# Kernel tuning notes

Hardware: AMD Instinct MI355X
Metric: run time of the kernel (lower is better)

## Reference

```python
import jax, jax.numpy as jnp
import numpy as np

B, SQ, SKV, D = 16, 2048, 2048, 128


def setup_inputs() -> dict:
    key = jax.random.key(0)
    kq, kk, kv = jax.random.split(key, 3)
    q = jax.random.normal(kq, (B, SQ, D), dtype=jnp.float32)
    k = jax.random.normal(kk, (B, SKV, D), dtype=jnp.float32)
    v = jax.random.normal(kv, (B, SKV, D), dtype=jnp.float32)
    return {"q": q, "k": k, "v": v, "dropout_p": 0}


def reference(q, k, v, dropout_p):
    # scores = q @ k^T, scaled by 1/sqrt(d)
    scale = 1.0 / np.sqrt(q.shape[-1]).astype(np.float32)
    scores = jnp.einsum('bqd,bkd->bqk', q, k) * scale  # [B, SQ, SKV]
    attn = jax.nn.softmax(scores, axis=-1)
    # dropout with p=dropout_p (0 here -> identity; deterministic baseline)
    if dropout_p > 0:
        keep = 1.0 - dropout_p
        mask = jax.random.bernoulli(jax.random.key(42), keep, attn.shape)
        attn = jnp.where(mask, attn / keep, 0.0)
    return jnp.einsum('bqk,bkd->bqd', attn, v)
```

## Files before the change

### kernel.cpp

```cpp
#include <hip/hip_runtime.h>
#include <hip/hip_bf16.h>
#include <cstdint>
#include <cmath>

#define SQL 2048
#define SKVL 2048
#define DD 128
#define NB 16
#define QBLK 64
#define KVB 32
#define NT 32

typedef __attribute__((ext_vector_type(8))) short short8;
typedef __attribute__((ext_vector_type(4))) float f32x4;

__device__ __forceinline__ ushort f2bf(float x) {
    union { float f; uint32_t u; } v; v.f = x;
    uint32_t r = v.u + 0x7FFFu + ((v.u >> 16) & 1u);
    return (ushort)(r >> 16);
}

__global__ void convert_scale_k(const float* __restrict__ in, ushort* __restrict__ out, float scale) {
    size_t i = (size_t)blockIdx.x * blockDim.x + threadIdx.x;
    const f32x4* p = (const f32x4*)in + i * 2;
    f32x4 a = p[0], b = p[1];
    short8 o;
    o[0] = (short)f2bf(a[0] * scale);
    o[1] = (short)f2bf(a[1] * scale);
    o[2] = (short)f2bf(a[2] * scale);
    o[3] = (short)f2bf(a[3] * scale);
    o[4] = (short)f2bf(b[0] * scale);
    o[5] = (short)f2bf(b[1] * scale);
    o[6] = (short)f2bf(b[2] * scale);
    o[7] = (short)f2bf(b[3] * scale);
    *((short8*)out + i) = o;
}

__global__ void convert_k_tiled(const float* __restrict__ in, ushort* __restrict__ out) {
    int gid = blockIdx.x * blockDim.x + threadIdx.x;
    int c16 = gid & 15;
    int rg  = gid >> 4;
    int r   = rg & 31;
    int tile = rg >> 5;
    const f32x4* p = (const f32x4*)(in + (size_t)rg * DD + c16 * 8);
    f32x4 a = p[0], b = p[1];
    short8 o;
    o[0] = (short)f2bf(a[0]); o[1] = (short)f2bf(a[1]);
    o[2] = (short)f2bf(a[2]); o[3] = (short)f2bf(a[3]);
    o[4] = (short)f2bf(b[0]); o[5] = (short)f2bf(b[1]);
    o[6] = (short)f2bf(b[2]); o[7] = (short)f2bf(b[3]);
    int cs = c16 ^ (r & 7);
    *(short8*)(out + ((size_t)tile << 12) + r * 128 + cs * 8) = o;
}

__global__ void convert_vt_tiled(const float* __restrict__ v, ushort* __restrict__ vt) {
    __shared__ float tile[32][129];
    int bid = blockIdx.x;
    int kt = bid & 63;
    int b  = bid >> 6;
    int tx = threadIdx.x;
    const float* src = v + ((size_t)b * SKVL + (size_t)kt * 32) * DD;
#pragma unroll
    for (int i = 0; i < 16; ++i) {
        int e = i * 256 + tx;
        tile[e >> 7][e & 127] = src[e];
    }
    __syncthreads();
    ushort* dst = vt + ((size_t)bid << 12);
#pragma unroll
    for (int i = 0; i < 2; ++i) {
        int q = i * 256 + tx;
        int d = q >> 2;
        int csp = q & 3;
        int cs = csp ^ ((d >> 1) & 3);
        short8 o;
#pragma unroll
        for (int j = 0; j < 8; ++j) {
            int kv = (j >> 2) * 16 + cs * 4 + (j & 3);
            o[j] = (short)f2bf(tile[kv][d]);
        }
        *(short8*)(dst + d * 32 + csp * 8) = o;
    }
}

#define GLD_LDS16(gsrc, ldst) \
    __builtin_amdgcn_global_load_lds((const __attribute__((address_space(1))) uint32_t*)(gsrc), \
                                     (__attribute__((address_space(3))) uint32_t*)(ldst), 16, 0, 0)

__global__ __launch_bounds__(256, 2) void fattn(
    const ushort* __restrict__ qb, const ushort* __restrict__ kbt,
    const ushort* __restrict__ vbt, float* __restrict__ out)
{
    __shared__ short8 kls[2][2][512];
    __shared__ short8 vls[2][2][512];

    int bid = blockIdx.x;
    int swz = (bid & 7) * 64 + (bid >> 3);
    int b  = swz >> 5;
    int qt = swz & 31;
    int lane = threadIdx.x & 63;
    int w = threadIdx.x >> 6;
    int g = lane >> 4;
    int qi = lane & 15;
    int rx = qi & 7;
    int vx = g ^ ((qi >> 1) & 3);
    int qrow = qt * QBLK + w * 16 + qi;

    const char* kA = (const char*)(kbt + ((size_t)(b * 64) << 12));
    const char* vA = (const char*)(vbt + ((size_t)(b * 64) << 12));
    const char* kB = kA + ((size_t)NT << 13);
    const char* vB = vA + ((size_t)NT << 13);

    const ushort* qptr = qb + ((size_t)b * SQL + qrow) * DD;
    short8 qf[4];
#pragma unroll
    for (int ks = 0; ks < 4; ++ks)
        qf[ks] = *(const short8*)(qptr + ks * 32 + g * 8);

    f32x4 accA[8], accB[8];
#pragma unroll
    for (int i = 0; i < 8; ++i) { accA[i] = (f32x4)0.f; accB[i] = (f32x4)0.f; }
    float mA = -1e30f, lA = 0.f, mB = -1e30f, lB = 0.f;

#pragma unroll
    for (int i = 0; i < 2; ++i) {
        int off = w * 2048 + i * 1024;
        GLD_LDS16(kA + off + lane * 16, (char*)&kls[0][0][0] + off);
        GLD_LDS16(vA + off + lane * 16, (char*)&vls[0][0][0] + off);
        GLD_LDS16(kB + off + lane * 16, (char*)&kls[1][0][0] + off);
        GLD_LDS16(vB + off + lane * 16, (char*)&vls[1][0][0] + off);
    }
    __syncthreads();

    for (int t = 0; t < NT; ++t) {
        int cur = t & 1, nxt = cur ^ 1;
        if (t + 1 < NT) {
            size_t toff = (size_t)(t + 1) << 13;
#pragma unroll
            for (int i = 0; i < 2; ++i) {
                int off = w * 2048 + i * 1024;
                GLD_LDS16(kA + toff + off + lane * 16, (char*)&kls[0][nxt][0] + off);
                GLD_LDS16(vA + toff + off + lane * 16, (char*)&vls[0][nxt][0] + off);
                GLD_LDS16(kB + toff + off + lane * 16, (char*)&kls[1][nxt][0] + off);
                GLD_LDS16(vB + toff + off + lane * 16, (char*)&vls[1][nxt][0] + off);
            }
        }
#pragma unroll
        for (int s2 = 0; s2 < 2; ++s2) {
            f32x4* acc = s2 ? accB : accA;
            float& m = s2 ? mB : mA;
            float& lsum = s2 ? lB : lA;
            f32x4 st[2];
            __builtin_amdgcn_s_setprio(1);
#pragma unroll
            for (int sub = 0; sub < 2; ++sub) {
                f32x4 s = (f32x4)0.f;
                int r = sub * 16 + qi;
#pragma unroll
                for (int ks = 0; ks < 4; ++ks) {
                    short8 kf = kls[s2][cur][r * 16 + ((ks * 4 + g) ^ rx)];
                    s = __builtin_amdgcn_mfma_f32_16x16x32_bf16(kf, qf[ks], s, 0, 0, 0);
                }
                st[sub] = s;
            }
            __builtin_amdgcn_s_setprio(0);
            float m0 = fmaxf(fmaxf(st[0][0], st[0][1]), fmaxf(st[0][2], st[0][3]));
            float m1 = fmaxf(fmaxf(st[1][0], st[1][1]), fmaxf(st[1][2], st[1][3]));
            float vmax = fmaxf(m0, m1);
            if (__any(vmax > m + 11.5f)) {
                float tmax = fmaxf(vmax, __shfl_xor(vmax, 16));
                tmax = fmaxf(tmax, __shfl_xor(tmax, 32));
                float mnew = fmaxf(m, tmax);
                float alpha = exp2f(m - mnew);
                m = mnew;
                lsum *= alpha;
#pragma unroll
                for (int i = 0; i < 8; ++i) {
                    acc[i][0] *= alpha; acc[i][1] *= alpha;
                    acc[i][2] *= alpha; acc[i][3] *= alpha;
                }
            }
            float pvv[8];
#pragma unroll
            for (int s = 0; s < 2; ++s) {
                pvv[s * 4 + 0] = exp2f(st[s][0] - m);
                pvv[s * 4 + 1] = exp2f(st[s][1] - m);
                pvv[s * 4 + 2] = exp2f(st[s][2] - m);
                pvv[s * 4 + 3] = exp2f(st[s][3] - m);
            }
            lsum += ((pvv[0] + pvv[1]) + (pvv[2] + pvv[3])) + ((pvv[4] + pvv[5]) + (pvv[6] + pvv[7]));
            union { short8 v; uint32_t u[4]; } P;
#pragma unroll
            for (int i = 0; i < 4; ++i)
                asm("v_cvt_pk_bf16_f32 %0, %1, %2" : "=v"(P.u[i]) : "v"(pvv[2 * i]), "v"(pvv[2 * i + 1]));
            __builtin_amdgcn_s_setprio(1);
#pragma unroll
            for (int dt = 0; dt < 8; ++dt) {
                int d = dt * 16 + qi;
                acc[dt] = __builtin_amdgcn_mfma_f32_16x16x32_bf16(
                    vls[s2][cur][d * 4 + vx], P.v, acc[dt], 0, 0, 0);
            }
            __builtin_amdgcn_s_setprio(0);
        }
        __syncthreads();
    }

    float mf = fmaxf(mA, mB);
    float fa = exp2f(mA - mf), fb = exp2f(mB - mf);
    float l = lA * fa + lB * fb;
    l += __shfl_xor(l, 16);
    l += __shfl_xor(l, 32);
    float inv = 1.f / l;
    float fia = fa * inv, fib = fb * inv;
    float* optr = out + ((size_t)b * SQL + qrow) * DD + g * 4;
#pragma unroll
    for (int dt = 0; dt < 8; ++dt) {
        f32x4 o;
        o[0] = accA[dt][0] * fia + accB[dt][0] * fib;
        o[1] = accA[dt][1] * fia + accB[dt][1] * fib;
        o[2] = accA[dt][2] * fia + accB[dt][2] * fib;
        o[3] = accA[dt][3] * fia + accB[dt][3] * fib;
        *(f32x4*)(optr + dt * 16) = o;
    }
}

extern "C" void kernel_launch(void* const* d_in, const int* in_sizes, int n_in,
                              void* d_out, int out_size, void* d_ws, size_t ws_size,
                              hipStream_t stream) {
    const float* q = (const float*)d_in[0];
    const float* k = (const float*)d_in[1];
    const float* v = (const float*)d_in[2];
    float* out = (float*)d_out;

    uint8_t* w = (uint8_t*)d_ws;
    size_t tsz = (size_t)NB * SQL * DD * sizeof(ushort);
    ushort* qb  = (ushort*)w;
    ushort* kbt = (ushort*)(w + tsz);
    ushort* vbt = (ushort*)(w + 2 * tsz);

    float qscale = 1.4426950408889634f / sqrtf((float)DD);
    int n8 = NB * SQL * DD / 8;
    convert_scale_k<<<n8 / 256, 256, 0, stream>>>(q, qb, qscale);
    convert_k_tiled<<<NB * SKVL * 16 / 256, 256, 0, stream>>>(k, kbt);
    convert_vt_tiled<<<NB * (SKVL / 32), 256, 0, stream>>>(v, vbt);
    fattn<<<NB * (SQL / QBLK), 256, 0, stream>>>(qb, kbt, vbt, out);
}
```

Baseline: 155.8 us.

## Split KV halves across separate warp groups with 512-thread blocks and LDS merge

```diff
diff --git a/kernel.cpp b/kernel.cpp
--- a/kernel.cpp
+++ b/kernel.cpp
@@ -87,7 +87,7 @@
     __builtin_amdgcn_global_load_lds((const __attribute__((address_space(1))) uint32_t*)(gsrc), \
                                      (__attribute__((address_space(3))) uint32_t*)(ldst), 16, 0, 0)
 
-__global__ __launch_bounds__(256, 2) void fattn(
+__global__ __launch_bounds__(512, 4) void fattn(
     const ushort* __restrict__ qb, const ushort* __restrict__ kbt,
     const ushort* __restrict__ vbt, float* __restrict__ out)
 {
@@ -100,16 +100,26 @@
     int qt = swz & 31;
     int lane = threadIdx.x & 63;
     int w = threadIdx.x >> 6;
+    int s2 = w >> 2;
+    int qg = w & 3;
     int g = lane >> 4;
     int qi = lane & 15;
     int rx = qi & 7;
     int vx = g ^ ((qi >> 1) & 3);
-    int qrow = qt * QBLK + w * 16 + qi;
-
-    const char* kA = (const char*)(kbt + ((size_t)(b * 64) << 12));
-    const char* vA = (const char*)(vbt + ((size_t)(b * 64) << 12));
-    const char* kB = kA + ((size_t)NT << 13);
-    const char* vB = vA + ((size_t)NT << 13);
+    int qrow = qt * QBLK + qg * 16 + qi;
+
+    const char* kS0 = (const char*)(kbt + ((size_t)(b * 64) << 12));
+    const char* vS0 = (const char*)(vbt + ((size_t)(b * 64) << 12));
+    const char* kS1 = kS0 + ((size_t)NT << 13);
+    const char* vS1 = vS0 + ((size_t)NT << 13);
+
+    int rreg = w >> 1;
+    const char* gbase = (rreg == 0) ? kS0 : (rreg == 1) ? vS0 : (rreg == 2) ? kS1 : vS1;
+    char* l0 = (rreg == 0) ? (char*)kls[0][0] : (rreg == 1) ? (char*)vls[0][0]
+             : (rreg == 2) ? (char*)kls[1][0] : (char*)vls[1][0];
+    char* l1 = (rreg == 0) ? (char*)kls[0][1] : (rreg == 1) ? (char*)vls[0][1]
+             : (rreg == 2) ? (char*)kls[1][1] : (char*)vls[1][1];
+    int soff = (w & 1) * 4096;
 
     const ushort* qptr = qb + ((size_t)b * SQL + qrow) * DD;
     short8 qf[4];
@@ -117,110 +127,115 @@
     for (int ks = 0; ks < 4; ++ks)
         qf[ks] = *(const short8*)(qptr + ks * 32 + g * 8);
 
-    f32x4 accA[8], accB[8];
-#pragma unroll
-    for (int i = 0; i < 8; ++i) { accA[i] = (f32x4)0.f; accB[i] = (f32x4)0.f; }
-    float mA = -1e30f, lA = 0.f, mB = -1e30f, lB = 0.f;
-
-#pragma unroll
-    for (int i = 0; i < 2; ++i) {
-        int off = w * 2048 + i * 1024;
-        GLD_LDS16(kA + off + lane * 16, (char*)&kls[0][0][0] + off);
-        GLD_LDS16(vA + off + lane * 16, (char*)&vls[0][0][0] + off);
-        GLD_LDS16(kB + off + lane * 16, (char*)&kls[1][0][0] + off);
-        GLD_LDS16(vB + off + lane * 16, (char*)&vls[1][0][0] + off);
-    }
+    f32x4 acc[8];
+#pragma unroll
+    for (int i = 0; i < 8; ++i) acc[i] = (f32x4)0.f;
+    float m = -1e30f, lsum = 0.f;
+
+#pragma unroll
+    for (int i = 0; i < 4; ++i)
+        GLD_LDS16(gbase + soff + i * 1024 + lane * 16, l0 + soff + i * 1024);
     __syncthreads();
+
+    const short8* kst = kls[s2][0];
+    const short8* vst = vls[s2][0];
 
     for (int t = 0; t < NT; ++t) {
         int cur = t & 1, nxt = cur ^ 1;
         if (t + 1 < NT) {
             size_t toff = (size_t)(t + 1) << 13;
-#pragma unroll
-            for (int i = 0; i < 2; ++i) {
-                int off = w * 2048 + i * 1024;
-                GLD_LDS16(kA + toff + off + lane * 16, (char*)&kls[0][nxt][0] + off);
-                GLD_LDS16(vA + toff + off + lane * 16, (char*)&vls[0][nxt][0] + off);
-                GLD_LDS16(kB + toff + off + lane * 16, (char*)&kls[1][nxt][0] + off);
-                GLD_LDS16(vB + toff + off + lane * 16, (char*)&vls[1][nxt][0] + off);
+            char* ld = nxt ? l1 : l0;
+#pragma unroll
+            for (int i = 0; i < 4; ++i)
+                GLD_LDS16(gbase + toff + soff + i * 1024 + lane * 16, ld + soff + i * 1024);
+        }
+        const short8* kcur = kst + cur * 512;
+        const short8* vcur = vst + cur * 512;
+        f32x4 st[2];
+        __builtin_amdgcn_s_setprio(1);
+#pragma unroll
+        for (int sub = 0; sub < 2; ++sub) {
+            f32x4 s = (f32x4)0.f;
+            int r = sub * 16 + qi;
+#pragma unroll
+            for (int ks = 0; ks < 4; ++ks) {
+                short8 kf = kcur[r * 16 + ((ks * 4 + g) ^ rx)];
+                s = __builtin_amdgcn_mfma_f32_16x16x32_bf16(kf, qf[ks], s, 0, 0, 0);
             }
-        }
-#pragma unroll
-        for (int s2 = 0; s2 < 2; ++s2) {
-            f32x4* acc = s2 ? accB : accA;
-            float& m = s2 ? mB : mA;
-            float& lsum = s2 ? lB : lA;
-            f32x4 st[2];
-            __builtin_amdgcn_s_setprio(1);
-#pragma unroll
-            for (int sub = 0; sub < 2; ++sub) {
-                f32x4 s = (f32x4)0.f;
-                int r = sub * 16 + qi;
-#pragma unroll
-                for (int ks = 0; ks < 4; ++ks) {
-                    short8 kf = kls[s2][cur][r * 16 + ((ks * 4 + g) ^ rx)];
-                    s = __builtin_amdgcn_mfma_f32_16x16x32_bf16(kf, qf[ks], s, 0, 0, 0);
-                }
-                st[sub] = s;
+            st[sub] = s;
+        }
+        __builtin_amdgcn_s_setprio(0);
+        float m0 = fmaxf(fmaxf(st[0][0], st[0][1]), fmaxf(st[0][2], st[0][3]));
+        float m1 = fmaxf(fmaxf(st[1][0], st[1][1]), fmaxf(st[1][2], st[1][3]));
+        float vmax = fmaxf(m0, m1);
+        if (__any(vmax > m + 11.5f)) {
+            float tmax = fmaxf(vmax, __shfl_xor(vmax, 16));
+            tmax = fmaxf(tmax, __shfl_xor(tmax, 32));
+            float mnew = fmaxf(m, tmax);
+            float alpha = exp2f(m - mnew);
+            m = mnew;
+            lsum *= alpha;
+#pragma unroll
+            for (int i = 0; i < 8; ++i) {
+                acc[i][0] *= alpha; acc[i][1] *= alpha;
+                acc[i][2] *= alpha; acc[i][3] *= alpha;
             }
-            __builtin_amdgcn_s_setprio(0);
-            float m0 = fmaxf(fmaxf(st[0][0], st[0][1]), fmaxf(st[0][2], st[0][3]));
-            float m1 = fmaxf(fmaxf(st[1][0], st[1][1]), fmaxf(st[1][2], st[1][3]));
-            float vmax = fmaxf(m0, m1);
-            if (__any(vmax > m + 11.5f)) {
-                float tmax = fmaxf(vmax, __shfl_xor(vmax, 16));
-                tmax = fmaxf(tmax, __shfl_xor(tmax, 32));
-                float mnew = fmaxf(m, tmax);
-                float alpha = exp2f(m - mnew);
-                m = mnew;
-                lsum *= alpha;
-#pragma unroll
-                for (int i = 0; i < 8; ++i) {
-                    acc[i][0] *= alpha; acc[i][1] *= alpha;
-                    acc[i][2] *= alpha; acc[i][3] *= alpha;
-                }
-            }
-            float pvv[8];
-#pragma unroll
-            for (int s = 0; s < 2; ++s) {
-                pvv[s * 4 + 0] = exp2f(st[s][0] - m);
-                pvv[s * 4 + 1] = exp2f(st[s][1] - m);
-                pvv[s * 4 + 2] = exp2f(st[s][2] - m);
-                pvv[s * 4 + 3] = exp2f(st[s][3] - m);
-            }
-            lsum += ((pvv[0] + pvv[1]) + (pvv[2] + pvv[3])) + ((pvv[4] + pvv[5]) + (pvv[6] + pvv[7]));
-            union { short8 v; uint32_t u[4]; } P;
-#pragma unroll
-            for (int i = 0; i < 4; ++i)
-                asm("v_cvt_pk_bf16_f32 %0, %1, %2" : "=v"(P.u[i]) : "v"(pvv[2 * i]), "v"(pvv[2 * i + 1]));
-            __builtin_amdgcn_s_setprio(1);
-#pragma unroll
-            for (int dt = 0; dt < 8; ++dt) {
-                int d = dt * 16 + qi;
-                acc[dt] = __builtin_amdgcn_mfma_f32_16x16x32_bf16(
-                    vls[s2][cur][d * 4 + vx], P.v, acc[dt], 0, 0, 0);
-            }
-            __builtin_amdgcn_s_setprio(0);
-        }
+        }
+        float pvv[8];
+#pragma unroll
+        for (int s = 0; s < 2; ++s) {
+            pvv[s * 4 + 0] = exp2f(st[s][0] - m);
+            pvv[s * 4 + 1] = exp2f(st[s][1] - m);
+            pvv[s * 4 + 2] = exp2f(st[s][2] - m);
+            pvv[s * 4 + 3] = exp2f(st[s][3] - m);
+        }
+        lsum += ((pvv[0] + pvv[1]) + (pvv[2] + pvv[3])) + ((pvv[4] + pvv[5]) + (pvv[6] + pvv[7]));
+        union { short8 v; uint32_t u[4]; } P;
+#pragma unroll
+        for (int i = 0; i < 4; ++i)
+            asm("v_cvt_pk_bf16_f32 %0, %1, %2" : "=v"(P.u[i]) : "v"(pvv[2 * i]), "v"(pvv[2 * i + 1]));
+        __builtin_amdgcn_s_setprio(1);
+#pragma unroll
+        for (int dt = 0; dt < 8; ++dt) {
+            int d = dt * 16 + qi;
+            acc[dt] = __builtin_amdgcn_mfma_f32_16x16x32_bf16(
+                vcur[d * 4 + vx], P.v, acc[dt], 0, 0, 0);
+        }
+        __builtin_amdgcn_s_setprio(0);
         __syncthreads();
     }
 
-    float mf = fmaxf(mA, mB);
-    float fa = exp2f(mA - mf), fb = exp2f(mB - mf);
-    float l = lA * fa + lB * fb;
-    l += __shfl_xor(l, 16);
-    l += __shfl_xor(l, 32);
-    float inv = 1.f / l;
-    float fia = fa * inv, fib = fb * inv;
-    float* optr = out + ((size_t)b * SQL + qrow) * DD + g * 4;
-#pragma unroll
-    for (int dt = 0; dt < 8; ++dt) {
-        f32x4 o;
-        o[0] = accA[dt][0] * fia + accB[dt][0] * fib;
-        o[1] = accA[dt][1] * fia + accB[dt][1] * fib;
-        o[2] = accA[dt][2] * fia + accB[dt][2] * fib;
-        o[3] = accA[dt][3] * fia + accB[dt][3] * fib;
-        *(f32x4*)(optr + dt * 16) = o;
+    float* mb = (float*)&kls[0][0][0];
+    if (w >= 4) {
+        int base = ((w - 4) * 64 + lane) * 36;
+#pragma unroll
+        for (int dt = 0; dt < 8; ++dt)
+            *(f32x4*)(mb + base + dt * 4) = acc[dt];
+        mb[base + 32] = m;
+        mb[base + 33] = lsum;
+    }
+    __syncthreads();
+    if (w < 4) {
+        int base = (w * 64 + lane) * 36;
+        float mB = mb[base + 32], lB = mb[base + 33];
+        float mf = fmaxf(m, mB);
+        float fa = exp2f(m - mf), fb = exp2f(mB - mf);
+        float l = lsum * fa + lB * fb;
+        l += __shfl_xor(l, 16);
+        l += __shfl_xor(l, 32);
+        float inv = 1.f / l;
+        float fia = fa * inv, fib = fb * inv;
+        float* optr = out + ((size_t)b * SQL + qrow) * DD + g * 4;
+#pragma unroll
+        for (int dt = 0; dt < 8; ++dt) {
+            f32x4 ob = *(const f32x4*)(mb + base + dt * 4);
+            f32x4 o;
+            o[0] = acc[dt][0] * fia + ob[0] * fib;
+            o[1] = acc[dt][1] * fia + ob[1] * fib;
+            o[2] = acc[dt][2] * fia + ob[2] * fib;
+            o[3] = acc[dt][3] * fia + ob[3] * fib;
+            *(f32x4*)(optr + dt * 16) = o;
+        }
     }
 }
 
@@ -243,5 +258,5 @@
     convert_scale_k<<<n8 / 256, 256, 0, stream>>>(q, qb, qscale);
     convert_k_tiled<<<NB * SKVL * 16 / 256, 256, 0, stream>>>(k, kbt);
     convert_vt_tiled<<<NB * (SKVL / 32), 256, 0, stream>>>(v, vbt);
-    fattn<<<NB * (SQL / QBLK), 256, 0, stream>>>(qb, kbt, vbt, out);
-}
+    fattn<<<NB * (SQL / QBLK), 512, 0, stream>>>(qb, kbt, vbt, out);
+}
```

Measured after the change: 149.2 us. 4.2% less time.

## Split KV sequence across four wave pairs with LDS merge of partial softmax

Applied to the files above, without the earlier changes.

```diff
diff --git a/kernel.cpp b/kernel.cpp
--- a/kernel.cpp
+++ b/kernel.cpp
@@ -9,7 +9,8 @@
 #define NB 16
 #define QBLK 64
 #define KVB 32
-#define NT 32
+#define NSTR 4
+#define NT 16
 
 typedef __attribute__((ext_vector_type(8))) short short8;
 typedef __attribute__((ext_vector_type(4))) float f32x4;
@@ -87,12 +88,13 @@
     __builtin_amdgcn_global_load_lds((const __attribute__((address_space(1))) uint32_t*)(gsrc), \
                                      (__attribute__((address_space(3))) uint32_t*)(ldst), 16, 0, 0)
 
-__global__ __launch_bounds__(256, 2) void fattn(
+__global__ __launch_bounds__(512, 4) void fattn(
     const ushort* __restrict__ qb, const ushort* __restrict__ kbt,
     const ushort* __restrict__ vbt, float* __restrict__ out)
 {
-    __shared__ short8 kls[2][2][512];
-    __shared__ short8 vls[2][2][512];
+    __shared__ char smem[65536];
+    short8* kls = (short8*)smem;
+    short8* vls = (short8*)(smem + 32768);
 
     int bid = blockIdx.x;
     int swz = (bid & 7) * 64 + (bid >> 3);
@@ -100,128 +102,162 @@
     int qt = swz & 31;
     int lane = threadIdx.x & 63;
     int w = threadIdx.x >> 6;
+    int s = w >> 1;
+    int qg = w & 1;
     int g = lane >> 4;
     int qi = lane & 15;
     int rx = qi & 7;
     int vx = g ^ ((qi >> 1) & 3);
-    int qrow = qt * QBLK + w * 16 + qi;
-
-    const char* kA = (const char*)(kbt + ((size_t)(b * 64) << 12));
-    const char* vA = (const char*)(vbt + ((size_t)(b * 64) << 12));
-    const char* kB = kA + ((size_t)NT << 13);
-    const char* vB = vA + ((size_t)NT << 13);
-
-    const ushort* qptr = qb + ((size_t)b * SQL + qrow) * DD;
-    short8 qf[4];
-#pragma unroll
-    for (int ks = 0; ks < 4; ++ks)
-        qf[ks] = *(const short8*)(qptr + ks * 32 + g * 8);
-
-    f32x4 accA[8], accB[8];
-#pragma unroll
-    for (int i = 0; i < 8; ++i) { accA[i] = (f32x4)0.f; accB[i] = (f32x4)0.f; }
-    float mA = -1e30f, lA = 0.f, mB = -1e30f, lB = 0.f;
-
-#pragma unroll
-    for (int i = 0; i < 2; ++i) {
-        int off = w * 2048 + i * 1024;
-        GLD_LDS16(kA + off + lane * 16, (char*)&kls[0][0][0] + off);
-        GLD_LDS16(vA + off + lane * 16, (char*)&vls[0][0][0] + off);
-        GLD_LDS16(kB + off + lane * 16, (char*)&kls[1][0][0] + off);
-        GLD_LDS16(vB + off + lane * 16, (char*)&vls[1][0][0] + off);
-    }
+
+    const short8* kl = kls + s * 512;
+    const short8* vl = vls + s * 512;
+    const ushort* kb_s = kbt + ((size_t)(b * 64 + s * 16) << 12);
+    const ushort* vb_s = vbt + ((size_t)(b * 64 + s * 16) << 12);
+    const char* gsrc = qg ? (const char*)vb_s : (const char*)kb_s;
+    char* ldst = qg ? (char*)(vls + s * 512) : (char*)(kls + s * 512);
+
+#define STAGE(t) do { const char* _g = gsrc + ((size_t)(t) << 13); \
+    _Pragma("unroll") for (int _i = 0; _i < 8; ++_i) \
+        GLD_LDS16(_g + _i * 1024 + lane * 16, ldst + _i * 1024); } while (0)
+
+    const ushort* qptr = qb + ((size_t)b * SQL + qt * QBLK + qg * 32 + qi) * DD;
+    short8 qf[2][4];
+#pragma unroll
+    for (int sub = 0; sub < 2; ++sub)
+#pragma unroll
+        for (int ks = 0; ks < 4; ++ks)
+            qf[sub][ks] = *(const short8*)(qptr + sub * 16 * DD + ks * 32 + g * 8);
+
+    f32x4 acc[2][8];
+#pragma unroll
+    for (int sub = 0; sub < 2; ++sub)
+#pragma unroll
+        for (int i = 0; i < 8; ++i) acc[sub][i] = (f32x4)0.f;
+    float m[2] = {-1e30f, -1e30f}, lsum[2] = {0.f, 0.f};
+
+    STAGE(0);
     __syncthreads();
 
     for (int t = 0; t < NT; ++t) {
-        int cur = t & 1, nxt = cur ^ 1;
-        if (t + 1 < NT) {
-            size_t toff = (size_t)(t + 1) << 13;
-#pragma unroll
-            for (int i = 0; i < 2; ++i) {
-                int off = w * 2048 + i * 1024;
-                GLD_LDS16(kA + toff + off + lane * 16, (char*)&kls[0][nxt][0] + off);
-                GLD_LDS16(vA + toff + off + lane * 16, (char*)&vls[0][nxt][0] + off);
-                GLD_LDS16(kB + toff + off + lane * 16, (char*)&kls[1][nxt][0] + off);
-                GLD_LDS16(vB + toff + off + lane * 16, (char*)&vls[1][nxt][0] + off);
-            }
-        }
-#pragma unroll
-        for (int s2 = 0; s2 < 2; ++s2) {
-            f32x4* acc = s2 ? accB : accA;
-            float& m = s2 ? mB : mA;
-            float& lsum = s2 ? lB : lA;
-            f32x4 st[2];
-            __builtin_amdgcn_s_setprio(1);
-#pragma unroll
-            for (int sub = 0; sub < 2; ++sub) {
-                f32x4 s = (f32x4)0.f;
-                int r = sub * 16 + qi;
-#pragma unroll
-                for (int ks = 0; ks < 4; ++ks) {
-                    short8 kf = kls[s2][cur][r * 16 + ((ks * 4 + g) ^ rx)];
-                    s = __builtin_amdgcn_mfma_f32_16x16x32_bf16(kf, qf[ks], s, 0, 0, 0);
+        f32x4 st0[2], st1[2];
+        __builtin_amdgcn_s_setprio(1);
+#pragma unroll
+        for (int kvs = 0; kvs < 2; ++kvs) {
+            f32x4 a0 = (f32x4)0.f, a1 = (f32x4)0.f;
+            int r = kvs * 16 + qi;
+#pragma unroll
+            for (int ks = 0; ks < 4; ++ks) {
+                short8 kf = kl[r * 16 + ((ks * 4 + g) ^ rx)];
+                a0 = __builtin_amdgcn_mfma_f32_16x16x32_bf16(kf, qf[0][ks], a0, 0, 0, 0);
+                a1 = __builtin_amdgcn_mfma_f32_16x16x32_bf16(kf, qf[1][ks], a1, 0, 0, 0);
+            }
+            st0[kvs] = a0; st1[kvs] = a1;
+        }
+        __builtin_amdgcn_s_setprio(0);
+        float vm0 = fmaxf(fmaxf(fmaxf(st0[0][0], st0[0][1]), fmaxf(st0[0][2], st0[0][3])),
+                          fmaxf(fmaxf(st0[1][0], st0[1][1]), fmaxf(st0[1][2], st0[1][3])));
+        float vm1 = fmaxf(fmaxf(fmaxf(st1[0][0], st1[0][1]), fmaxf(st1[0][2], st1[0][3])),
+                          fmaxf(fmaxf(st1[1][0], st1[1][1]), fmaxf(st1[1][2], st1[1][3])));
+        if (__any((vm0 > m[0] + 11.5f) || (vm1 > m[1] + 11.5f))) {
+            float t0 = fmaxf(vm0, __shfl_xor(vm0, 16)); t0 = fmaxf(t0, __shfl_xor(t0, 32));
+            float t1 = fmaxf(vm1, __shfl_xor(vm1, 16)); t1 = fmaxf(t1, __shfl_xor(t1, 32));
+            float mn0 = fmaxf(m[0], t0), mn1 = fmaxf(m[1], t1);
+            float a0 = exp2f(m[0] - mn0), a1 = exp2f(m[1] - mn1);
+            m[0] = mn0; m[1] = mn1;
+            lsum[0] *= a0; lsum[1] *= a1;
+#pragma unroll
+            for (int i = 0; i < 8; ++i) { acc[0][i] *= a0; acc[1][i] *= a1; }
+        }
+        union { short8 v; uint32_t u[4]; } P0, P1;
+        {
+            float pvv[8];
+#pragma unroll
+            for (int kvs = 0; kvs < 2; ++kvs) {
+                pvv[kvs * 4 + 0] = exp2f(st0[kvs][0] - m[0]);
+                pvv[kvs * 4 + 1] = exp2f(st0[kvs][1] - m[0]);
+                pvv[kvs * 4 + 2] = exp2f(st0[kvs][2] - m[0]);
+                pvv[kvs * 4 + 3] = exp2f(st0[kvs][3] - m[0]);
+            }
+            lsum[0] += ((pvv[0] + pvv[1]) + (pvv[2] + pvv[3])) + ((pvv[4] + pvv[5]) + (pvv[6] + pvv[7]));
+#pragma unroll
+            for (int i = 0; i < 4; ++i)
+                asm("v_cvt_pk_bf16_f32 %0, %1, %2" : "=v"(P0.u[i]) : "v"(pvv[2 * i]), "v"(pvv[2 * i + 1]));
+        }
+        {
+            float pvv[8];
+#pragma unroll
+            for (int kvs = 0; kvs < 2; ++kvs) {
+                pvv[kvs * 4 + 0] = exp2f(st1[kvs][0] - m[1]);
+                pvv[kvs * 4 + 1] = exp2f(st1[kvs][1] - m[1]);
+                pvv[kvs * 4 + 2] = exp2f(st1[kvs][2] - m[1]);
+                pvv[kvs * 4 + 3] = exp2f(st1[kvs][3] - m[1]);
+            }
+            lsum[1] += ((pvv[0] + pvv[1]) + (pvv[2] + pvv[3])) + ((pvv[4] + pvv[5]) + (pvv[6] + pvv[7]));
+#pragma unroll
+            for (int i = 0; i < 4; ++i)
+                asm("v_cvt_pk_bf16_f32 %0, %1, %2" : "=v"(P1.u[i]) : "v"(pvv[2 * i]), "v"(pvv[2 * i + 1]));
+        }
+        __builtin_amdgcn_s_setprio(1);
+#pragma unroll
+        for (int dt = 0; dt < 8; ++dt) {
+            short8 vf = vl[(dt * 16 + qi) * 4 + vx];
+            acc[0][dt] = __builtin_amdgcn_mfma_f32_16x16x32_bf16(vf, P0.v, acc[0][dt], 0, 0, 0);
+            acc[1][dt] = __builtin_amdgcn_mfma_f32_16x16x32_bf16(vf, P1.v, acc[1][dt], 0, 0, 0);
+        }
+        __builtin_amdgcn_s_setprio(0);
+        __syncthreads();
+        if (t + 1 < NT) STAGE(t + 1);
+        __syncthreads();
+    }
+
+    float* mb = (float*)smem;
+#pragma unroll 2
+    for (int sub = 0; sub < 2; ++sub) {
+        __syncthreads();
+        if (s > 0) {
+            float* dst = mb + (((qg * 3) + (s - 1)) * 64 + lane) * 36;
+#pragma unroll
+            for (int dt = 0; dt < 8; ++dt)
+                *(f32x4*)(dst + dt * 4) = acc[sub][dt];
+            dst[32] = m[sub];
+            dst[33] = lsum[sub];
+        }
+        __syncthreads();
+        if (s == 0) {
+#pragma unroll
+            for (int ps = 0; ps < 3; ++ps) {
+                const float* src = mb + (((qg * 3) + ps) * 64 + lane) * 36;
+                float mp = src[32], lp = src[33];
+                float mf = fmaxf(m[sub], mp);
+                float fa = exp2f(m[sub] - mf), fp = exp2f(mp - mf);
+                m[sub] = mf;
+                lsum[sub] = lsum[sub] * fa + lp * fp;
+#pragma unroll
+                for (int dt = 0; dt < 8; ++dt) {
+                    f32x4 ap = *(const f32x4*)(src + dt * 4);
+                    acc[sub][dt] = acc[sub][dt] * fa + ap * fp;
                 }
-                st[sub] = s;
-            }
-            __builtin_amdgcn_s_setprio(0);
-            float m0 = fmaxf(fmaxf(st[0][0], st[0][1]), fmaxf(st[0][2], st[0][3]));
-            float m1 = fmaxf(fmaxf(st[1][0], st[1][1]), fmaxf(st[1][2], st[1][3]));
-            float vmax = fmaxf(m0, m1);
-            if (__any(vmax > m + 11.5f)) {
-                float tmax = fmaxf(vmax, __shfl_xor(vmax, 16));
-                tmax = fmaxf(tmax, __shfl_xor(tmax, 32));
-                float mnew = fmaxf(m, tmax);
-                float alpha = exp2f(m - mnew);
-                m = mnew;
-                lsum *= alpha;
-#pragma unroll
-                for (int i = 0; i < 8; ++i) {
-                    acc[i][0] *= alpha; acc[i][1] *= alpha;
-                    acc[i][2] *= alpha; acc[i][3] *= alpha;
-                }
-            }
-            float pvv[8];
-#pragma unroll
-            for (int s = 0; s < 2; ++s) {
-                pvv[s * 4 + 0] = exp2f(st[s][0] - m);
-                pvv[s * 4 + 1] = exp2f(st[s][1] - m);
-                pvv[s * 4 + 2] = exp2f(st[s][2] - m);
-                pvv[s * 4 + 3] = exp2f(st[s][3] - m);
-            }
-            lsum += ((pvv[0] + pvv[1]) + (pvv[2] + pvv[3])) + ((pvv[4] + pvv[5]) + (pvv[6] + pvv[7]));
-            union { short8 v; uint32_t u[4]; } P;
-#pragma unroll
-            for (int i = 0; i < 4; ++i)
-                asm("v_cvt_pk_bf16_f32 %0, %1, %2" : "=v"(P.u[i]) : "v"(pvv[2 * i]), "v"(pvv[2 * i + 1]));
-            __builtin_amdgcn_s_setprio(1);
+            }
+        }
+    }
+    if (s == 0) {
+#pragma unroll 2
+        for (int sub = 0; sub < 2; ++sub) {
+            float l = lsum[sub];
+            l += __shfl_xor(l, 16);
+            l += __shfl_xor(l, 32);
+            float inv = 1.f / l;
+            float* optr = out + ((size_t)b * SQL + qt * QBLK + qg * 32 + sub * 16 + qi) * DD + g * 4;
 #pragma unroll
             for (int dt = 0; dt < 8; ++dt) {
-                int d = dt * 16 + qi;
-                acc[dt] = __builtin_amdgcn_mfma_f32_16x16x32_bf16(
-                    vls[s2][cur][d * 4 + vx], P.v, acc[dt], 0, 0, 0);
-            }
-            __builtin_amdgcn_s_setprio(0);
-        }
-        __syncthreads();
-    }
-
-    float mf = fmaxf(mA, mB);
-    float fa = exp2f(mA - mf), fb = exp2f(mB - mf);
-    float l = lA * fa + lB * fb;
-    l += __shfl_xor(l, 16);
-    l += __shfl_xor(l, 32);
-    float inv = 1.f / l;
-    float fia = fa * inv, fib = fb * inv;
-    float* optr = out + ((size_t)b * SQL + qrow) * DD + g * 4;
-#pragma unroll
-    for (int dt = 0; dt < 8; ++dt) {
-        f32x4 o;
-        o[0] = accA[dt][0] * fia + accB[dt][0] * fib;
-        o[1] = accA[dt][1] * fia + accB[dt][1] * fib;
-        o[2] = accA[dt][2] * fia + accB[dt][2] * fib;
-        o[3] = accA[dt][3] * fia + accB[dt][3] * fib;
-        *(f32x4*)(optr + dt * 16) = o;
-    }
+                f32x4 o;
+                o[0] = acc[sub][dt][0] * inv; o[1] = acc[sub][dt][1] * inv;
+                o[2] = acc[sub][dt][2] * inv; o[3] = acc[sub][dt][3] * inv;
+                *(f32x4*)(optr + dt * 16) = o;
+            }
+        }
+    }
+#undef STAGE
 }
 
 extern "C" void kernel_launch(void* const* d_in, const int* in_sizes, int n_in,
@@ -243,5 +279,5 @@
     convert_scale_k<<<n8 / 256, 256, 0, stream>>>(q, qb, qscale);
     convert_k_tiled<<<NB * SKVL * 16 / 256, 256, 0, stream>>>(k, kbt);
     convert_vt_tiled<<<NB * (SKVL / 32), 256, 0, stream>>>(v, vbt);
-    fattn<<<NB * (SQL / QBLK), 256, 0, stream>>>(qb, kbt, vbt, out);
-}
+    fattn<<<NB * (SQL / QBLK), 512, 0, stream>>>(qb, kbt, vbt, out);
+}
```

After: 178.7 us. 1.15x slower.
